# Performance work log

Hardware: AMD Instinct MI355X
Metric: run time of the kernel (lower is better)

## Reference

```python
import jax, jax.numpy as jnp
import numpy as np

B, M, L, HID, H, LAYERS = 16, 128, 512, 256, 4, 2
DH = HID // H  # 64 = head dim, also kernel_param dim


def _ln(x, g, b, eps=1e-5):
    mu = jnp.mean(x, axis=-1, keepdims=True)
    var = jnp.mean((x - mu) ** 2, axis=-1, keepdims=True)
    return (x - mu) / jnp.sqrt(var + eps) * g + b


def setup_inputs() -> dict:
    key = jax.random.key(0)
    ks = jax.random.split(key, 24)
    s = 0.05
    return {
        "ct_t": jax.random.uniform(ks[0], (B, M), jnp.float32),
        "ts_t": jax.random.uniform(ks[1], (B, L), jnp.float32),
        "ct_emb": jax.random.normal(ks[2], (B, M, HID), jnp.float32),
        "ts_emb": jax.random.normal(ks[3], (B, L, HID), jnp.float32),
        "kernel_param": jax.random.normal(ks[4], (DH,), jnp.float32),
        "ct_W": jax.random.normal(ks[5], (HID, HID), jnp.float32) * s,
        "ct_b": jnp.zeros((HID,), jnp.float32),
        "fW0": jax.random.normal(ks[6], (HID, HID), jnp.float32) * s,
        "fb0": jnp.zeros((HID,), jnp.float32),
        "fW1": jax.random.normal(ks[7], (HID, HID), jnp.float32) * s,
        "fb1": jnp.zeros((HID,), jnp.float32),
        "fW2": jax.random.normal(ks[8], (HID, HID), jnp.float32) * s,
        "fb2": jnp.zeros((HID,), jnp.float32),
        "f_ln_g": jnp.ones((HID,), jnp.float32),
        "f_ln_b": jnp.zeros((HID,), jnp.float32),
        "Wqkv": jax.random.normal(ks[9], (LAYERS, 3 * HID, HID), jnp.float32) * s,
        "bqkv": jnp.zeros((LAYERS, 3 * HID), jnp.float32),
        "Wo": jax.random.normal(ks[10], (LAYERS, HID, HID), jnp.float32) * s,
        "bo": jnp.zeros((LAYERS, HID), jnp.float32),
        "W1": jax.random.normal(ks[11], (LAYERS, 2 * HID, HID), jnp.float32) * s,
        "b1": jnp.zeros((LAYERS, 2 * HID), jnp.float32),
        "W2": jax.random.normal(ks[12], (LAYERS, HID, 2 * HID), jnp.float32) * s,
        "b2": jnp.zeros((LAYERS, HID), jnp.float32),
        "ln1_g": jnp.ones((LAYERS, HID), jnp.float32),
        "ln1_b": jnp.zeros((LAYERS, HID), jnp.float32),
        "ln2_g": jnp.ones((LAYERS, HID), jnp.float32),
        "ln2_b": jnp.zeros((LAYERS, HID), jnp.float32),
        "pred_W": jax.random.normal(ks[13], (1, HID), jnp.float32) * s,
        "pred_b": jnp.zeros((1,), jnp.float32),
    }


def reference(ct_t, ts_t, ct_emb, ts_emb, kernel_param, ct_W, ct_b,
              fW0, fb0, fW1, fb1, fW2, fb2, f_ln_g, f_ln_b,
              Wqkv, bqkv, Wo, bo, W1, b1, W2, b2,
              ln1_g, ln1_b, ln2_g, ln2_b, pred_W, pred_b):
    # --- TN tokenizer: multi-scale RBF kernel temporal fusion ---
    alpha = jax.nn.softplus(kernel_param)                       # [DH]  log(1+exp(p))
    ct_e = (jnp.einsum('bmd,ed->bme', ct_emb, ct_W) + ct_b)     # [B,M,HID]
    ct_e = ct_e.reshape(B, M, H, DH)
    diff = ct_t[:, :, None] - ts_t[:, None, :]                  # [B,M,L]
    norm = (diff * diff)[..., None]                             # [B,M,L,1]
    outs = []
    for s in range(H):                                          # fixed small loop over scales
        z = (-float(s)) * alpha * norm                          # [B,M,L,DH]
        w = jax.nn.logsumexp(z, axis=3, keepdims=True)          # [B,M,L,1]
        sim = jnp.exp(z - w)                                    # normalized kernel sims
        outs.append(jnp.einsum('bmnd,bmd->bnd', sim, ct_e[:, :, s, :]))  # scatter over ts events
    temp = jnp.concatenate(outs, axis=-1)                       # [B,L,HID]
    # --- Fusion module ---
    aux = jax.nn.elu(temp @ fW0.T + fb0 + ts_emb @ fW1.T + fb1)
    x = _ln(aux @ fW2.T + fb2 + ts_emb, f_ln_g, f_ln_b)         # [B,L,HID]
    # --- Transformer encoder (post-LN, gelu, no dropout at eval) ---
    inv_sqrt = 1.0 / np.sqrt(DH).astype(np.float32)
    for l in range(LAYERS):
        qkv = x @ Wqkv[l].T + bqkv[l]                           # [B,L,3*HID]
        q, k, v = jnp.split(qkv, 3, axis=-1)
        def heads(t):
            return t.reshape(B, L, H, DH).transpose(0, 2, 1, 3)
        q, k, v = heads(q), heads(k), heads(v)
        att = jax.nn.softmax(jnp.einsum('bhqd,bhkd->bhqk', q, k) * inv_sqrt, axis=-1)
        o = jnp.einsum('bhqk,bhkd->bhqd', att, v).transpose(0, 2, 1, 3).reshape(B, L, HID)
        x = _ln(x + o @ Wo[l].T + bo[l], ln1_g[l], ln1_b[l])
        ff = jax.nn.gelu(x @ W1[l].T + b1[l], approximate=False) @ W2[l].T + b2[l]
        x = _ln(x + ff, ln2_g[l], ln2_b[l])
    return x @ pred_W.T + pred_b                                # [B,L,1]
```

## Files before the change

kernel.cpp:

```cpp
#include <hip/hip_runtime.h>
#include <hip/hip_bf16.h>
#include <cstddef>

#define Bsz 16
#define Msz 128
#define Lsz 512
#define HIDs 256

typedef __attribute__((ext_vector_type(4))) float f32x4;
typedef __attribute__((ext_vector_type(8))) __bf16 bf16x8;
typedef __attribute__((ext_vector_type(8))) unsigned short ushort8;

#define CHEB_K 12
#define PI_F 3.14159265358979323846f

static __device__ inline unsigned short f2bf(float f) {
    __hip_bfloat16 h = __float2bfloat16(f);
    return *(unsigned short*)&h;
}
static __device__ inline float bf2f(unsigned short u) {
    return __builtin_bit_cast(float, (unsigned)u << 16);
}
static __device__ inline void gload16(const ushort* g, ushort* l) {
    __builtin_amdgcn_global_load_lds(
        (const __attribute__((address_space(1))) void*)g,
        (__attribute__((address_space(3))) void*)l, 16, 0, 0);
}

__global__ __launch_bounds__(256) void cheb_kernel(
    const float* __restrict__ kp, float* __restrict__ clut, float* __restrict__ cD)
{
    __shared__ float costab[CHEB_K][32];
    __shared__ float xq[32];
    __shared__ float alph[64];
    const int t = threadIdx.x;
    if (t < 64) {
        float p = kp[t];
        alph[t] = fmaxf(p, 0.f) + log1pf(__expf(-fabsf(p)));
    }
    #pragma unroll
    for (int i = 0; i < 2; i++) {
        int idx = i * 256 + t;
        if (idx < CHEB_K * 32) {
            int k = idx >> 5, q = idx & 31;
            float th = (q + 0.5f) * (PI_F / 32.f);
            costab[k][q] = __cosf((float)k * th);
        }
    }
    if (t < 32) xq[t] = 0.5f * (1.f + __cosf((t + 0.5f) * (PI_F / 32.f)));
    __syncthreads();

    if (t >= 192) return;
    const int d = t & 63, s1 = t >> 6;
    const float u = (float)(s1 + 1) * alph[d];
    float f[32];
    #pragma unroll
    for (int q = 0; q < 32; q++) f[q] = __expf(-u * xq[q]);
    #pragma unroll
    for (int k = 0; k < CHEB_K; k++) {
        float sum = 0.f;
        #pragma unroll
        for (int q = 0; q < 32; q++) sum = fmaf(f[q], costab[k][q], sum);
        float c = sum * ((k == 0 ? 1.f : 2.f) / 32.f);
        clut[s1 * (CHEB_K * 64) + k * 64 + d] = c;
        float sr = c;
        #pragma unroll
        for (int o = 1; o <= 32; o <<= 1) sr += __shfl_xor(sr, o, 64);
        if (d == 0) cD[s1 * CHEB_K + k] = sr;
    }
}

__global__ __launch_bounds__(256) void prep_kernel(
    const float* __restrict__ ts_emb, const float* __restrict__ ct_emb,
    const float* __restrict__ ct_W, const float* __restrict__ fW0,
    const float* __restrict__ fW1, const float* __restrict__ fW2,
    const float* __restrict__ Wqkv, const float* __restrict__ Wo,
    const float* __restrict__ W1, const float* __restrict__ W2,
    ushort* __restrict__ Xcat, ushort* __restrict__ Wcat,
    ushort* __restrict__ cebin, ushort* __restrict__ wct,
    ushort* __restrict__ wf2, ushort* __restrict__ wqkv,
    ushort* __restrict__ wo, ushort* __restrict__ w1, ushort* __restrict__ w2,
    const float* __restrict__ ct_t, const float* __restrict__ ts_t,
    const float* __restrict__ cD, ushort* __restrict__ invW,
    const float* __restrict__ bqkv, float* __restrict__ bqs)
{
    const int bid = blockIdx.x;
    const int tid = threadIdx.x;

    if (bid < 1920) {
        const unsigned u = bid * 256u + tid;
        const float* src; ushort* dst; unsigned rel;
        float sc = 1.f;
        if (u < 262144u) {
            rel = u; src = ts_emb;
            dst = Xcat + ((size_t)(rel >> 5) * 512 + 256 + (rel & 31) * 8);
        } else if (u < 327680u) { rel = u - 262144u; src = ct_emb; dst = cebin + (size_t)rel * 8; }
        else if (u < 335872u) { rel = u - 327680u; src = ct_W; dst = wct + (size_t)rel * 8; }
        else if (u < 344064u) { rel = u - 335872u; src = fW0;
            dst = Wcat + ((size_t)(rel >> 5) * 512 + (rel & 31) * 8); }
        else if (u < 352256u) { rel = u - 344064u; src = fW1;
            dst = Wcat + ((size_t)(rel >> 5) * 512 + 256 + (rel & 31) * 8); }
        else if (u < 360448u) { rel = u - 352256u; src = fW2; dst = wf2 + (size_t)rel * 8; }
        else if (u < 409600u) { rel = u - 360448u; src = Wqkv; dst = wqkv + (size_t)rel * 8;
            if (((rel >> 5) % 768) < 256) sc = 0.125f; }
        else if (u < 425984u) { rel = u - 409600u; src = Wo;  dst = wo + (size_t)rel * 8; }
        else if (u < 458752u) { rel = u - 425984u; src = W1;  dst = w1 + (size_t)rel * 8; }
        else                  { rel = u - 458752u; src = W2;  dst = w2 + (size_t)rel * 8; }
        float4 a = ((const float4*)src)[(size_t)rel * 2];
        float4 b = ((const float4*)src)[(size_t)rel * 2 + 1];
        ushort8 o;
        o[0] = f2bf(a.x * sc); o[1] = f2bf(a.y * sc); o[2] = f2bf(a.z * sc); o[3] = f2bf(a.w * sc);
        o[4] = f2bf(b.x * sc); o[5] = f2bf(b.y * sc); o[6] = f2bf(b.z * sc); o[7] = f2bf(b.w * sc);
        *(ushort8*)dst = o;
    } else if (bid < 6016) {
        __shared__ float cd[3][CHEB_K];
        if (tid < 3 * CHEB_K) cd[tid / CHEB_K][tid % CHEB_K] = cD[tid];
        __syncthreads();

        const unsigned G = (bid - 1920) * 256u + tid;
        const int b = G >> 16;
        const int n = (G >> 7) & 511;
        const int m = G & 127;

        float x = ct_t[b * Msz + m] - ts_t[b * Lsz + n];
        x = x * x;
        const float xi = 2.f * x - 1.f;
        const float xi2 = 2.f * xi;

        float t0 = 1.f, t1 = xi;
        float a1 = cd[0][0] + cd[0][1] * xi;
        float a2 = cd[1][0] + cd[1][1] * xi;
        float a3 = cd[2][0] + cd[2][1] * xi;
        #pragma unroll
        for (int k = 2; k < CHEB_K; k++) {
            float tn = fmaf(xi2, t1, -t0);
            a1 = fmaf(cd[0][k], tn, a1);
            a2 = fmaf(cd[1][k], tn, a2);
            a3 = fmaf(cd[2][k], tn, a3);
            t0 = t1; t1 = tn;
        }
        const size_t base = ((size_t)b * 3 * Lsz + n) * Msz + m;
        invW[base]                         = f2bf(1.f / a1);
        invW[base + (size_t)Lsz * Msz]     = f2bf(1.f / a2);
        invW[base + (size_t)2 * Lsz * Msz] = f2bf(1.f / a3);
    } else {
        #pragma unroll
        for (int i = 0; i < 6; i++) {
            int idx = i * 256 + tid;
            int c = idx % 768;
            bqs[idx] = bqkv[idx] * ((c < 256) ? 0.125f : 1.f);
        }
    }
}

__global__ __launch_bounds__(256) void gemm_mfma_kernel(
    const ushort* __restrict__ X, const ushort* __restrict__ W,
    const float* __restrict__ bias, const float* __restrict__ bias2,
    ushort* __restrict__ Yb, int NR, int K, int OUT, int act)
{
    __shared__ ushort As[2][64 * 64];
    __shared__ ushort Bs[2][128 * 64];

    const int nbx = OUT >> 7;
    const int bx = blockIdx.x % nbx;
    const int by = blockIdx.x / nbx;
    const int r0 = by << 6, o0 = bx << 7;
    const int tid = threadIdx.x;
    const int w = tid >> 6;
    const int lane = tid & 63;
    const int wr = w >> 1, wc = w & 1;
    const int lr = lane & 15, lg = lane >> 4;

    const int grow = lane >> 3;
    const int gchunk = (lane & 7) ^ grow;

    unsigned aoff[2][2], boff[4][2];
    #pragma unroll
    for (int f = 0; f < 2; f++) {
        unsigned cc = (unsigned)((lg + 4 * f) ^ (lr & 7)) * 16u;
        #pragma unroll
        for (int m = 0; m < 2; m++)
            aoff[m][f] = (unsigned)(wr * 32 + m * 16 + lr) * 128u + cc;
        #pragma unroll
        for (int n = 0; n < 4; n++)
            boff[n][f] = (unsigned)(wc * 64 + n * 16 + lr) * 128u + cc;
    }

    f32x4 acc[2][4];
    #pragma unroll
    for (int m = 0; m < 2; m++)
        #pragma unroll
        for (int n = 0; n < 4; n++) acc[m][n] = (f32x4){0.f, 0.f, 0.f, 0.f};

    const int nk = K >> 6;

    auto stage = [&](int buf, int ks) {
        const int k0 = ks << 6;
        #pragma unroll
        for (int i = 0; i < 2; i++) {
            int row = w * 16 + i * 8 + grow;
            gload16(X + (size_t)(r0 + row) * K + k0 + gchunk * 8,
                    &As[buf][(w * 16 + i * 8) * 64]);
        }
        #pragma unroll
        for (int i = 0; i < 4; i++) {
            int row = w * 32 + i * 8 + grow;
            gload16(W + (size_t)(o0 + row) * K + k0 + gchunk * 8,
                    &Bs[buf][(w * 32 + i * 8) * 64]);
        }
    };

    stage(0, 0);
    __syncthreads();
    int cur = 0;
    for (int ks = 0; ks < nk; ks++) {
        if (ks + 1 < nk) stage(cur ^ 1, ks + 1);
        const char* Ab = (const char*)As[cur];
        const char* Bb = (const char*)Bs[cur];
        #pragma unroll
        for (int f = 0; f < 2; f++) {
            bf16x8 av[2], bv[4];
            #pragma unroll
            for (int m = 0; m < 2; m++)
                av[m] = *(const bf16x8*)(Ab + aoff[m][f]);
            #pragma unroll
            for (int n = 0; n < 4; n++)
                bv[n] = *(const bf16x8*)(Bb + boff[n][f]);
            #pragma unroll
            for (int m = 0; m < 2; m++)
                #pragma unroll
                for (int n = 0; n < 4; n++)
                    acc[m][n] = __builtin_amdgcn_mfma_f32_16x16x32_bf16(
                        av[m], bv[n], acc[m][n], 0, 0, 0);
        }
        __syncthreads();
        cur ^= 1;
    }

    const int ocol0 = o0 + wc * 64;
    float bn[4];
    #pragma unroll
    for (int n = 0; n < 4; n++) {
        int o = ocol0 + n * 16 + lr;
        bn[n] = bias[o] + (bias2 ? bias2[o] : 0.f);
    }

    #pragma unroll
    for (int m = 0; m < 2; m++) {
        #pragma unroll
        for (int p = 0; p < 4; p++) {
            int r = r0 + wr * 32 + m * 16 + 4 * lg + p;
            size_t rb = (size_t)r * OUT;
            #pragma unroll
            for (int n = 0; n < 4; n++) {
                int o = ocol0 + n * 16 + lr;
                float v = acc[m][n][p] + bn[n];
                if (act == 1)      v = (v > 0.f) ? v : (__expf(v) - 1.f);
                else if (act == 2) v = 0.5f * v * (1.f + erff(v * 0.70710678118654752f));
                Yb[rb + o] = f2bf(v);
            }
        }
    }
}

__global__ __launch_bounds__(512) void gemm_ln_kernel(
    const ushort* __restrict__ X, const ushort* __restrict__ W,
    const float* __restrict__ bias, const ushort* __restrict__ add,
    int addS, int addO,
    const float* __restrict__ lng, const float* __restrict__ lnb,
    ushort* __restrict__ Xb,
    const float* __restrict__ predW, const float* __restrict__ predb,
    float* __restrict__ pout, int K)
{
    __shared__ ushort As[2][32 * 64];
    __shared__ ushort Bs[2][256 * 64];
    __shared__ float redA[32][4];
    __shared__ float redB[32][4];

    const int r0 = blockIdx.x << 5;
    const int tid = threadIdx.x;
    const int w = tid >> 6;
    const int lane = tid & 63;
    const int lr = lane & 15, lg = lane >> 4;
    const int wg = w >> 2;
    const int ws = w & 3;
    const int grow = lane >> 3;
    const int gchunk = (lane & 7) ^ grow;

    unsigned aoff[2], boff[4][2];
    #pragma unroll
    for (int f = 0; f < 2; f++) {
        unsigned cc = (unsigned)((lg + 4 * f) ^ (lr & 7)) * 16u;
        aoff[f] = (unsigned)(wg * 16 + lr) * 128u + cc;
        #pragma unroll
        for (int n = 0; n < 4; n++)
            boff[n][f] = (unsigned)(ws * 64 + n * 16 + lr) * 128u + cc;
    }

    f32x4 acc[4];
    #pragma unroll
    for (int n = 0; n < 4; n++) acc[n] = (f32x4){0.f, 0.f, 0.f, 0.f};

    const int nk = K >> 6;

    auto stage = [&](int buf, int ks) {
        const int k0 = ks << 6;
        if (w < 4)
            gload16(X + (size_t)(r0 + w * 8 + grow) * K + k0 + gchunk * 8,
                    &As[buf][(w * 8) * 64]);
        #pragma unroll
        for (int i = 0; i < 4; i++) {
            gload16(W + (size_t)(w * 32 + i * 8 + grow) * K + k0 + gchunk * 8,
                    &Bs[buf][(w * 32 + i * 8) * 64]);
        }
    };

    stage(0, 0);
    __syncthreads();
    int cur = 0;
    for (int ks = 0; ks < nk; ks++) {
        if (ks + 1 < nk) stage(cur ^ 1, ks + 1);
        const char* Ab = (const char*)As[cur];
        const char* Bb = (const char*)Bs[cur];
        #pragma unroll
        for (int f = 0; f < 2; f++) {
            bf16x8 av = *(const bf16x8*)(Ab + aoff[f]);
            #pragma unroll
            for (int n = 0; n < 4; n++) {
                bf16x8 bv = *(const bf16x8*)(Bb + boff[n][f]);
                acc[n] = __builtin_amdgcn_mfma_f32_16x16x32_bf16(
                    av, bv, acc[n], 0, 0, 0);
            }
        }
        __syncthreads();
        cur ^= 1;
    }

    const int col0 = ws * 64;
    float bn[4], gv[4], bv2[4], pwv[4];
    #pragma unroll
    for (int n = 0; n < 4; n++) {
        int o = col0 + n * 16 + lr;
        bn[n] = bias[o];
        gv[n] = lng[o];
        bv2[n] = lnb[o];
        pwv[n] = predW ? predW[o] : 0.f;
    }
    #pragma unroll
    for (int p = 0; p < 4; p++) {
        size_t ra = (size_t)(r0 + wg * 16 + 4 * lg + p) * addS + addO;
        #pragma unroll
        for (int n = 0; n < 4; n++)
            acc[n][p] += bn[n] + bf2f(add[ra + col0 + n * 16 + lr]);
    }

    #pragma unroll
    for (int p = 0; p < 4; p++) {
        float s = acc[0][p] + acc[1][p] + acc[2][p] + acc[3][p];
        #pragma unroll
        for (int o = 1; o <= 8; o <<= 1) s += __shfl_xor(s, o);
        if (lr == 0) redA[wg * 16 + 4 * lg + p][ws] = s;
    }
    __syncthreads();
    float mu[4];
    #pragma unroll
    for (int p = 0; p < 4; p++) {
        int row = wg * 16 + 4 * lg + p;
        mu[p] = (redA[row][0] + redA[row][1] + redA[row][2] + redA[row][3]) * (1.f / 256.f);
    }

    #pragma unroll
    for (int p = 0; p < 4; p++) {
        float q = 0.f;
        #pragma unroll
        for (int n = 0; n < 4; n++) {
            float dl = acc[n][p] - mu[p];
            q = fmaf(dl, dl, q);
        }
        #pragma unroll
        for (int o = 1; o <= 8; o <<= 1) q += __shfl_xor(q, o);
        if (lr == 0) redB[wg * 16 + 4 * lg + p][ws] = q;
    }
    __syncthreads();

    #pragma unroll
    for (int p = 0; p < 4; p++) {
        int row = wg * 16 + 4 * lg + p;
        float var = (redB[row][0] + redB[row][1] + redB[row][2] + redB[row][3]) * (1.f / 256.f);
        float rsig = rsqrtf(var + 1e-5f);
        size_t rb = (size_t)(r0 + row) * 256;
        float pd = 0.f;
        #pragma unroll
        for (int n = 0; n < 4; n++) {
            int o = col0 + n * 16 + lr;
            float xn = (acc[n][p] - mu[p]) * rsig * gv[n] + bv2[n];
            if (Xb) Xb[rb + o] = f2bf(xn);
            pd = fmaf(xn, pwv[n], pd);
        }
        if (predW) {
            #pragma unroll
            for (int o = 1; o <= 8; o <<= 1) pd += __shfl_xor(pd, o);
            if (lr == 0) redA[row][ws] = pd;
        }
    }
    if (predW) {
        __syncthreads();
        if (tid < 32)
            pout[r0 + tid] = redA[tid][0] + redA[tid][1] + redA[tid][2]
                           + redA[tid][3] + predb[0];
    }
}

__global__ __launch_bounds__(256) void tokmix_kernel(
    const float* __restrict__ ct_t, const float* __restrict__ ts_t,
    const ushort* __restrict__ ceb, const ushort* __restrict__ invW,
    const float* __restrict__ clut, ushort* __restrict__ Xcat)
{
    const int bid = blockIdx.x;
    const int tid = threadIdx.x;

    if (bid < 384) {
        const int nt = bid & 7;
        const int s1 = (bid >> 3) % 3;
        const int b  = bid / 24;
        const int w = tid >> 6, lane = tid & 63, g = lane >> 4, r = lane & 15;

        __shared__ ushort ceT[64][136];
        __shared__ float  cl[CHEB_K][64];
        __shared__ float  cts[128];

        #pragma unroll
        for (int i = 0; i < 8; i++) {
            int idx = i * 256 + tid;
            int m = idx >> 4, d4 = (idx & 15) << 2;
            const ushort* gp = ceb + (((size_t)b * 128 + m) << 8) + (s1 + 1) * 64 + d4;
            ushort4 v = *(const ushort4*)gp;
            ceT[d4 + 0][m] = v.x; ceT[d4 + 1][m] = v.y;
            ceT[d4 + 2][m] = v.z; ceT[d4 + 3][m] = v.w;
        }
        #pragma unroll
        for (int i = 0; i < 3; i++) {
            int idx = i * 256 + tid;
            cl[idx >> 6][idx & 63] = clut[s1 * (CHEB_K * 64) + idx];
        }
        if (tid < 128) cts[tid] = ct_t[b * 128 + tid];
        __syncthreads();

        const int nrow = nt * 64 + w * 16 + r;
        const float tsn = ts_t[b * 512 + nrow];

        float xi2v[4][8], Ta[4][8], Tb[4][8];
        #pragma unroll
        for (int t4 = 0; t4 < 4; t4++) {
            int m0 = 8 * g + 32 * t4;
            ushort8 iv = *(const ushort8*)&invW[((((size_t)b * 3 + s1) * 512 + nrow) << 7) + m0];
            #pragma unroll
            for (int j = 0; j < 8; j++) {
                float dfx = cts[m0 + j] - tsn;
                float x = dfx * dfx;
                float xi = 2.f * x - 1.f;
                float w0 = bf2f(iv[j]);
                xi2v[t4][j] = 2.f * xi;
                Ta[t4][j] = w0;
                Tb[t4][j] = w0 * xi;
            }
        }

        bf16x8 cef[4][4];
        #pragma unroll
        for (int db = 0; db < 4; db++)
            #pragma unroll
            for (int t4 = 0; t4 < 4; t4++)
                cef[db][t4] = *(const bf16x8*)&ceT[db * 16 + r][8 * g + 32 * t4];

        f32x4 acc[4];
        #pragma unroll
        for (int db = 0; db < 4; db++) acc[db] = (f32x4){0.f, 0.f, 0.f, 0.f};

        #pragma unroll
        for (int k = 0; k < CHEB_K; k++) {
            if (k >= 2) {
                #pragma unroll
                for (int t4 = 0; t4 < 4; t4++)
                    #pragma unroll
                    for (int j = 0; j < 8; j++) {
                        if (k & 1) Tb[t4][j] = fmaf(xi2v[t4][j], Ta[t4][j], -Tb[t4][j]);
                        else       Ta[t4][j] = fmaf(xi2v[t4][j], Tb[t4][j], -Ta[t4][j]);
                    }
            }
            bf16x8 af[4];
            #pragma unroll
            for (int t4 = 0; t4 < 4; t4++) {
                ushort8 u;
                #pragma unroll
                for (int j = 0; j < 8; j++)
                    u[j] = f2bf((k & 1) ? Tb[t4][j] : Ta[t4][j]);
                af[t4] = __builtin_bit_cast(bf16x8, u);
            }
            #pragma unroll
            for (int db = 0; db < 4; db++) {
                f32x4 gk = (f32x4){0.f, 0.f, 0.f, 0.f};
                #pragma unroll
                for (int t4 = 0; t4 < 4; t4++)
                    gk = __builtin_amdgcn_mfma_f32_16x16x32_bf16(af[t4], cef[db][t4], gk, 0, 0, 0);
                float ck = cl[k][db * 16 + r];
                #pragma unroll
                for (int p = 0; p < 4; p++) acc[db][p] = fmaf(ck, gk[p], acc[db][p]);
            }
        }

        #pragma unroll
        for (int db = 0; db < 4; db++)
            #pragma unroll
            for (int p = 0; p < 4; p++) {
                int n_out = nt * 64 + w * 16 + 4 * g + p;
                Xcat[((size_t)b * 512 + n_out) * 512 + (s1 + 1) * 64 + db * 16 + r] =
                    f2bf(acc[db][p]);
            }
    } else {
        const int b = bid - 384;
        const int d = tid & 63, q = tid >> 6;
        float s = 0.f;
        #pragma unroll 8
        for (int i = 0; i < 32; i++) {
            int m = q * 32 + i;
            s += bf2f(ceb[(((size_t)b * 128 + m) << 8) + d]);
        }
        __shared__ float red0[4][64];
        __shared__ ushort row0[64];
        red0[q][d] = s;
        __syncthreads();
        if (tid < 64)
            row0[tid] = f2bf((red0[0][tid] + red0[1][tid] + red0[2][tid] + red0[3][tid])
                             * (1.f / 64.f));
        __syncthreads();
        #pragma unroll
        for (int i = 0; i < 16; i++) {
            int idx = i * 256 + tid;
            int n = idx >> 3, j = idx & 7;
            *(ushort8*)&Xcat[((size_t)b * 512 + n) * 512 + j * 8] =
                *(const ushort8*)&row0[j * 8];
        }
    }
}

__global__ __launch_bounds__(256) void attn_mfma_kernel(
    const ushort* __restrict__ qkv, ushort* __restrict__ Ob)
{
    const int bid = blockIdx.x;
    const int qt = bid & 7;
    const int h  = (bid >> 3) & 3;
    const int b  = bid >> 5;
    const int t  = threadIdx.x;
    const int w  = t >> 6;
    const int lane = t & 63;
    const int g = lane >> 4;
    const int r = lane & 15;

    __shared__ ushort Ks[128][72];
    __shared__ ushort Vt[64][136];
    __shared__ ushort Pb[4][16][136];

    const ushort* base = qkv + (size_t)b * Lsz * 768;
    const int q0 = qt * 64 + w * 16;

    bf16x8 qf[2];
    {
        const ushort* qp = base + (size_t)(q0 + r) * 768 + h * 64 + 8 * g;
        qf[0] = __builtin_bit_cast(bf16x8, *(const ushort8*)qp);
        qf[1] = __builtin_bit_cast(bf16x8, *(const ushort8*)(qp + 32));
    }

    f32x4 Ofr[4];
    #pragma unroll
    for (int dblk = 0; dblk < 4; dblk++) Ofr[dblk] = (f32x4){0.f, 0.f, 0.f, 0.f};
    float m_run[4] = {-1e30f, -1e30f, -1e30f, -1e30f};
    float l_run[4] = {0.f, 0.f, 0.f, 0.f};

    const int srow = t >> 1;
    const int sseg = t & 1;

    ushort8 pk[4], pv[4];
    auto gload_chunk = [&](int c) {
        const ushort* kr = base + (size_t)(c * 128 + srow) * 768 + 256 + h * 64 + sseg * 32;
        #pragma unroll
        for (int i = 0; i < 4; i++) {
            pk[i] = *(const ushort8*)(kr + 8 * i);
            pv[i] = *(const ushort8*)(kr + 256 + 8 * i);
        }
    };
    auto write_chunk = [&]() {
        #pragma unroll
        for (int i = 0; i < 4; i++) {
            *(ushort8*)&Ks[srow][sseg * 32 + 8 * i] = pk[i];
            #pragma unroll
            for (int j = 0; j < 8; j++)
                Vt[sseg * 32 + 8 * i + j][srow] = pv[i][j];
        }
    };

    gload_chunk(0);
    write_chunk();
    __syncthreads();

    for (int c = 0; c < 4; c++) {
        if (c < 3) gload_chunk(c + 1);

        f32x4 sfr[8];
        __builtin_amdgcn_s_setprio(1);
        #pragma unroll
        for (int s = 0; s < 8; s++) {
            f32x4 a2 = (f32x4){0.f, 0.f, 0.f, 0.f};
            #pragma unroll
            for (int f = 0; f < 2; f++) {
                bf16x8 kf = *(const bf16x8*)&Ks[s * 16 + r][8 * g + 32 * f];
                a2 = __builtin_amdgcn_mfma_f32_16x16x32_bf16(qf[f], kf, a2, 0, 0, 0);
            }
            sfr[s] = a2;
        }
        __builtin_amdgcn_s_setprio(0);

        #pragma unroll
        for (int p = 0; p < 4; p++) {
            float rm = sfr[0][p];
            #pragma unroll
            for (int s = 1; s < 8; s++) rm = fmaxf(rm, sfr[s][p]);
            #pragma unroll
            for (int o = 1; o <= 8; o <<= 1) rm = fmaxf(rm, __shfl_xor(rm, o));
            float mnew = fmaxf(m_run[p], rm);
            float sc = __expf(m_run[p] - mnew);
            m_run[p] = mnew;
            float rs = 0.f;
            #pragma unroll
            for (int s = 0; s < 8; s++) {
                float pvx = __expf(sfr[s][p] - mnew);
                Pb[w][4 * g + p][s * 16 + r] = f2bf(pvx);
                rs += pvx;
            }
            #pragma unroll
            for (int o = 1; o <= 8; o <<= 1) rs += __shfl_xor(rs, o);
            l_run[p] = l_run[p] * sc + rs;
            #pragma unroll
            for (int dblk = 0; dblk < 4; dblk++) Ofr[dblk][p] *= sc;
        }

        __asm__ volatile("s_waitcnt lgkmcnt(0)" ::: "memory");

        #pragma unroll
        for (int ks2 = 0; ks2 < 4; ks2++) {
            bf16x8 pa = *(const bf16x8*)&Pb[w][r][8 * g + 32 * ks2];
            __builtin_amdgcn_s_setprio(1);
            #pragma unroll
            for (int dblk = 0; dblk < 4; dblk++) {
                bf16x8 vb = *(const bf16x8*)&Vt[dblk * 16 + r][32 * ks2 + 8 * g];
                Ofr[dblk] = __builtin_amdgcn_mfma_f32_16x16x32_bf16(
                    pa, vb, Ofr[dblk], 0, 0, 0);
            }
            __builtin_amdgcn_s_setprio(0);
        }

        __syncthreads();
        if (c < 3) {
            write_chunk();
            __syncthreads();
        }
    }

    #pragma unroll
    for (int dblk = 0; dblk < 4; dblk++) {
        #pragma unroll
        for (int p = 0; p < 4; p++) {
            int row = q0 + 4 * g + p;
            Ob[(size_t)(b * Lsz + row) * HIDs + h * 64 + dblk * 16 + r] =
                f2bf(Ofr[dblk][p] / l_run[p]);
        }
    }
}

extern "C" void kernel_launch(void* const* d_in, const int* in_sizes, int n_in,
                              void* d_out, int out_size, void* d_ws, size_t ws_size,
                              hipStream_t stream)
{
    (void)in_sizes; (void)n_in; (void)out_size; (void)ws_size;

    const float* ct_t   = (const float*)d_in[0];
    const float* ts_t   = (const float*)d_in[1];
    const float* ct_emb = (const float*)d_in[2];
    const float* ts_emb = (const float*)d_in[3];
    const float* kp     = (const float*)d_in[4];
    const float* ct_W   = (const float*)d_in[5];
    const float* ct_b   = (const float*)d_in[6];
    const float* fW0    = (const float*)d_in[7];
    const float* fb0    = (const float*)d_in[8];
    const float* fW1    = (const float*)d_in[9];
    const float* fb1    = (const float*)d_in[10];
    const float* fW2    = (const float*)d_in[11];
    const float* fb2    = (const float*)d_in[12];
    const float* f_ln_g = (const float*)d_in[13];
    const float* f_ln_b = (const float*)d_in[14];
    const float* Wqkv   = (const float*)d_in[15];
    const float* bqkv   = (const float*)d_in[16];
    const float* Wo     = (const float*)d_in[17];
    const float* bo     = (const float*)d_in[18];
    const float* W1     = (const float*)d_in[19];
    const float* b1     = (const float*)d_in[20];
    const float* W2     = (const float*)d_in[21];
    const float* b2     = (const float*)d_in[22];
    const float* ln1_g  = (const float*)d_in[23];
    const float* ln1_b  = (const float*)d_in[24];
    const float* ln2_g  = (const float*)d_in[25];
    const float* ln2_b  = (const float*)d_in[26];
    const float* pred_W = (const float*)d_in[27];
    const float* pred_b = (const float*)d_in[28];

    ushort* wsb = (ushort*)d_ws;
    ushort* invW  = wsb;
    ushort* auxbf = wsb;
    ushort* qkvbf = wsb;
    ushort* ff1bf = wsb;
    ushort* Xcat  = wsb + 12582912;
    ushort* Wcat  = wsb + 16777216;
    ushort* cebin = wsb + 16908288;
    ushort* cebout= wsb + 17432576;
    ushort* wct   = wsb + 17956864;
    ushort* wf2   = wsb + 18022400;
    ushort* wqkv  = wsb + 18087936;
    ushort* wo    = wsb + 18481152;
    ushort* w1    = wsb + 18612224;
    ushort* w2    = wsb + 18874368;
    ushort* xbf   = wsb + 19136512;
    ushort* obf   = wsb + 21233664;
    float*  wsf   = (float*)d_ws;
    float*  clut  = wsf + 11665408;
    float*  cDp   = wsf + 11667712;
    float*  bqs   = wsf + 11667776;

    const int NRts = Bsz * Lsz;
    const int NRct = Bsz * Msz;
    auto grid = [](int nr, int out) { return dim3((unsigned)((nr >> 6) * (out >> 7))); };

    cheb_kernel<<<dim3(1), 256, 0, stream>>>(kp, clut, cDp);
    prep_kernel<<<dim3(1920 + 4096 + 1), 256, 0, stream>>>(
        ts_emb, ct_emb, ct_W, fW0, fW1, fW2, Wqkv, Wo, W1, W2,
        Xcat, Wcat, cebin, wct, wf2, wqkv, wo, w1, w2,
        ct_t, ts_t, cDp, invW, bqkv, bqs);

    gemm_mfma_kernel<<<grid(NRct, 256), 256, 0, stream>>>(
        cebin, wct, ct_b, nullptr, cebout, NRct, 256, 256, 0);
    tokmix_kernel<<<dim3(400), 256, 0, stream>>>(ct_t, ts_t, cebout, invW, clut, Xcat);

    gemm_mfma_kernel<<<grid(NRts, 256), 256, 0, stream>>>(
        Xcat, Wcat, fb0, fb1, auxbf, NRts, 512, 256, 1);
    gemm_ln_kernel<<<dim3(NRts / 32), 512, 0, stream>>>(
        auxbf, wf2, fb2, Xcat, 512, 256, f_ln_g, f_ln_b, xbf,
        nullptr, nullptr, nullptr, 256);

    for (int l = 0; l < 2; l++) {
        gemm_mfma_kernel<<<grid(NRts, 768), 256, 0, stream>>>(
            xbf, wqkv + (size_t)l * 196608, bqs + l * 768, nullptr,
            qkvbf, NRts, 256, 768, 0);
        attn_mfma_kernel<<<dim3(512), 256, 0, stream>>>(qkvbf, obf);
        gemm_ln_kernel<<<dim3(NRts / 32), 512, 0, stream>>>(
            obf, wo + (size_t)l * 65536, bo + l * 256, xbf, 256, 0,
            ln1_g + l * 256, ln1_b + l * 256, xbf,
            nullptr, nullptr, nullptr, 256);
        gemm_mfma_kernel<<<grid(NRts, 512), 256, 0, stream>>>(
            xbf, w1 + (size_t)l * 131072, b1 + l * 512, nullptr,
            ff1bf, NRts, 256, 512, 2);
        if (l == 0) {
            gemm_ln_kernel<<<dim3(NRts / 32), 512, 0, stream>>>(
                ff1bf, w2 + (size_t)l * 131072, b2 + l * 256, xbf, 256, 0,
                ln2_g + l * 256, ln2_b + l * 256, xbf,
                nullptr, nullptr, nullptr, 512);
        } else {
            gemm_ln_kernel<<<dim3(NRts / 32), 512, 0, stream>>>(
                ff1bf, w2 + (size_t)l * 131072, b2 + l * 256, xbf, 256, 0,
                ln2_g + l * 256, ln2_b + l * 256, nullptr,
                pred_W, pred_b, (float*)d_out, 512);
        }
    }
}
```

Measured before the change: 188.9 us.

## Fold Chebyshev coefficient kernel into consumers and use lazy softmax rescaling

Removes the single-block cheb_kernel launch and instead recomputes the Chebyshev coefficients inside prep_kernel (per block, in shared memory) and inside tokmix_kernel (per block, for its s1 slice). This drops one serial kernel launch and a global round trip, at the cost of redundant per-block transcendental and FMA work across about 4096 prep blocks and 384 tokmix blocks. Separately, the attention online softmax now rescales the running max, sum and output only when some row's new max exceeds the old one by more than 8, which saves exp and multiply work per tile. The exponentials can then grow up to e^8 and are stored in bf16, which is a numerical tradeoff.

```diff
diff --git a/kernel.cpp b/kernel.cpp
--- a/kernel.cpp
+++ b/kernel.cpp
@@ -25,49 +25,6 @@
     __builtin_amdgcn_global_load_lds(
         (const __attribute__((address_space(1))) void*)g,
         (__attribute__((address_space(3))) void*)l, 16, 0, 0);
-}
-
-__global__ __launch_bounds__(256) void cheb_kernel(
-    const float* __restrict__ kp, float* __restrict__ clut, float* __restrict__ cD)
-{
-    __shared__ float costab[CHEB_K][32];
-    __shared__ float xq[32];
-    __shared__ float alph[64];
-    const int t = threadIdx.x;
-    if (t < 64) {
-        float p = kp[t];
-        alph[t] = fmaxf(p, 0.f) + log1pf(__expf(-fabsf(p)));
-    }
-    #pragma unroll
-    for (int i = 0; i < 2; i++) {
-        int idx = i * 256 + t;
-        if (idx < CHEB_K * 32) {
-            int k = idx >> 5, q = idx & 31;
-            float th = (q + 0.5f) * (PI_F / 32.f);
-            costab[k][q] = __cosf((float)k * th);
-        }
-    }
-    if (t < 32) xq[t] = 0.5f * (1.f + __cosf((t + 0.5f) * (PI_F / 32.f)));
-    __syncthreads();
-
-    if (t >= 192) return;
-    const int d = t & 63, s1 = t >> 6;
-    const float u = (float)(s1 + 1) * alph[d];
-    float f[32];
-    #pragma unroll
-    for (int q = 0; q < 32; q++) f[q] = __expf(-u * xq[q]);
-    #pragma unroll
-    for (int k = 0; k < CHEB_K; k++) {
-        float sum = 0.f;
-        #pragma unroll
-        for (int q = 0; q < 32; q++) sum = fmaf(f[q], costab[k][q], sum);
-        float c = sum * ((k == 0 ? 1.f : 2.f) / 32.f);
-        clut[s1 * (CHEB_K * 64) + k * 64 + d] = c;
-        float sr = c;
-        #pragma unroll
-        for (int o = 1; o <= 32; o <<= 1) sr += __shfl_xor(sr, o, 64);
-        if (d == 0) cD[s1 * CHEB_K + k] = sr;
-    }
 }
 
 __global__ __launch_bounds__(256) void prep_kernel(
@@ -81,7 +38,7 @@
     ushort* __restrict__ wf2, ushort* __restrict__ wqkv,
     ushort* __restrict__ wo, ushort* __restrict__ w1, ushort* __restrict__ w2,
     const float* __restrict__ ct_t, const float* __restrict__ ts_t,
-    const float* __restrict__ cD, ushort* __restrict__ invW,
+    const float* __restrict__ kp, ushort* __restrict__ invW,
     const float* __restrict__ bqkv, float* __restrict__ bqs)
 {
     const int bid = blockIdx.x;
@@ -114,7 +71,37 @@
         *(ushort8*)dst = o;
     } else if (bid < 6016) {
         __shared__ float cd[3][CHEB_K];
-        if (tid < 3 * CHEB_K) cd[tid / CHEB_K][tid % CHEB_K] = cD[tid];
+        __shared__ float costab[CHEB_K][32];
+        __shared__ float xq[32];
+        #pragma unroll
+        for (int i = 0; i < 2; i++) {
+            int idx = i * 256 + tid;
+            if (idx < CHEB_K * 32) {
+                int k = idx >> 5, q = idx & 31;
+                costab[k][q] = __cosf((float)k * ((q + 0.5f) * (PI_F / 32.f)));
+            }
+        }
+        if (tid < 32) xq[tid] = 0.5f * (1.f + __cosf((tid + 0.5f) * (PI_F / 32.f)));
+        __syncthreads();
+        if (tid < 192) {
+            const int d = tid & 63, s1 = tid >> 6;
+            float p = kp[d];
+            float a = fmaxf(p, 0.f) + log1pf(__expf(-fabsf(p)));
+            const float u = (float)(s1 + 1) * a;
+            float f[32];
+            #pragma unroll
+            for (int q = 0; q < 32; q++) f[q] = __expf(-u * xq[q]);
+            #pragma unroll
+            for (int k = 0; k < CHEB_K; k++) {
+                float sum = 0.f;
+                #pragma unroll
+                for (int q = 0; q < 32; q++) sum = fmaf(f[q], costab[k][q], sum);
+                float c = sum * ((k == 0 ? 1.f : 2.f) / 32.f);
+                #pragma unroll
+                for (int o = 1; o <= 32; o <<= 1) c += __shfl_xor(c, o, 64);
+                if (d == 0) cd[s1][k] = c;
+            }
+        }
         __syncthreads();
 
         const unsigned G = (bid - 1920) * 256u + tid;
@@ -414,7 +401,7 @@
 __global__ __launch_bounds__(256) void tokmix_kernel(
     const float* __restrict__ ct_t, const float* __restrict__ ts_t,
     const ushort* __restrict__ ceb, const ushort* __restrict__ invW,
-    const float* __restrict__ clut, ushort* __restrict__ Xcat)
+    const float* __restrict__ kp, ushort* __restrict__ Xcat)
 {
     const int bid = blockIdx.x;
     const int tid = threadIdx.x;
@@ -428,6 +415,8 @@
         __shared__ ushort ceT[64][136];
         __shared__ float  cl[CHEB_K][64];
         __shared__ float  cts[128];
+        __shared__ float  costab[CHEB_K][32];
+        __shared__ float  xq[32];
 
         #pragma unroll
         for (int i = 0; i < 8; i++) {
@@ -439,12 +428,32 @@
             ceT[d4 + 2][m] = v.z; ceT[d4 + 3][m] = v.w;
         }
         #pragma unroll
-        for (int i = 0; i < 3; i++) {
+        for (int i = 0; i < 2; i++) {
             int idx = i * 256 + tid;
-            cl[idx >> 6][idx & 63] = clut[s1 * (CHEB_K * 64) + idx];
-        }
+            if (idx < CHEB_K * 32) {
+                int k = idx >> 5, q = idx & 31;
+                costab[k][q] = __cosf((float)k * ((q + 0.5f) * (PI_F / 32.f)));
+            }
+        }
+        if (tid < 32) xq[tid] = 0.5f * (1.f + __cosf((tid + 0.5f) * (PI_F / 32.f)));
         if (tid < 128) cts[tid] = ct_t[b * 128 + tid];
         __syncthreads();
+
+        if (tid < 64) {
+            float p = kp[tid];
+            float a = fmaxf(p, 0.f) + log1pf(__expf(-fabsf(p)));
+            const float u = (float)(s1 + 1) * a;
+            float f[32];
+            #pragma unroll
+            for (int q = 0; q < 32; q++) f[q] = __expf(-u * xq[q]);
+            #pragma unroll
+            for (int k = 0; k < CHEB_K; k++) {
+                float sum = 0.f;
+                #pragma unroll
+                for (int q = 0; q < 32; q++) sum = fmaf(f[q], costab[k][q], sum);
+                cl[k][tid] = sum * ((k == 0 ? 1.f : 2.f) / 32.f);
+            }
+        }
 
         const int nrow = nt * 64 + w * 16 + r;
         const float tsn = ts_t[b * 512 + nrow];
@@ -472,6 +481,8 @@
             #pragma unroll
             for (int t4 = 0; t4 < 4; t4++)
                 cef[db][t4] = *(const bf16x8*)&ceT[db * 16 + r][8 * g + 32 * t4];
+
+        __syncthreads();
 
         f32x4 acc[4];
         #pragma unroll
@@ -627,21 +638,24 @@
             for (int s = 1; s < 8; s++) rm = fmaxf(rm, sfr[s][p]);
             #pragma unroll
             for (int o = 1; o <= 8; o <<= 1) rm = fmaxf(rm, __shfl_xor(rm, o));
-            float mnew = fmaxf(m_run[p], rm);
-            float sc = __expf(m_run[p] - mnew);
-            m_run[p] = mnew;
+            if (__any(rm > m_run[p] + 8.f)) {
+                float mnew = fmaxf(m_run[p], rm);
+                float sc = __expf(m_run[p] - mnew);
+                m_run[p] = mnew;
+                l_run[p] *= sc;
+                #pragma unroll
+                for (int dblk = 0; dblk < 4; dblk++) Ofr[dblk][p] *= sc;
+            }
             float rs = 0.f;
             #pragma unroll
             for (int s = 0; s < 8; s++) {
-                float pvx = __expf(sfr[s][p] - mnew);
+                float pvx = __expf(sfr[s][p] - m_run[p]);
                 Pb[w][4 * g + p][s * 16 + r] = f2bf(pvx);
                 rs += pvx;
             }
             #pragma unroll
             for (int o = 1; o <= 8; o <<= 1) rs += __shfl_xor(rs, o);
-            l_run[p] = l_run[p] * sc + rs;
-            #pragma unroll
-            for (int dblk = 0; dblk < 4; dblk++) Ofr[dblk][p] *= sc;
+            l_run[p] += rs;
         }
 
         __asm__ volatile("s_waitcnt lgkmcnt(0)" ::: "memory");
@@ -731,23 +745,20 @@
     ushort* xbf   = wsb + 19136512;
     ushort* obf   = wsb + 21233664;
     float*  wsf   = (float*)d_ws;
-    float*  clut  = wsf + 11665408;
-    float*  cDp   = wsf + 11667712;
-    float*  bqs   = wsf + 11667776;
+    float*  bqs   = wsf + 11665408;
 
     const int NRts = Bsz * Lsz;
     const int NRct = Bsz * Msz;
     auto grid = [](int nr, int out) { return dim3((unsigned)((nr >> 6) * (out >> 7))); };
 
-    cheb_kernel<<<dim3(1), 256, 0, stream>>>(kp, clut, cDp);
     prep_kernel<<<dim3(1920 + 4096 + 1), 256, 0, stream>>>(
         ts_emb, ct_emb, ct_W, fW0, fW1, fW2, Wqkv, Wo, W1, W2,
         Xcat, Wcat, cebin, wct, wf2, wqkv, wo, w1, w2,
-        ct_t, ts_t, cDp, invW, bqkv, bqs);
+        ct_t, ts_t, kp, invW, bqkv, bqs);
 
     gemm_mfma_kernel<<<grid(NRct, 256), 256, 0, stream>>>(
         cebin, wct, ct_b, nullptr, cebout, NRct, 256, 256, 0);
-    tokmix_kernel<<<dim3(400), 256, 0, stream>>>(ct_t, ts_t, cebout, invW, clut, Xcat);
+    tokmix_kernel<<<dim3(400), 256, 0, stream>>>(ct_t, ts_t, cebout, invW, kp, Xcat);
 
     gemm_mfma_kernel<<<grid(NRts, 256), 256, 0, stream>>>(
         Xcat, Wcat, fb0, fb1, auxbf, NRts, 512, 256, 1);
```

After: 208.0 us. 1.1x slower.
